# Optimization experiments

Hardware: AMD Instinct MI355X
Metric: run time of the kernel (lower is better)

Reference implementation:

```python
import jax, jax.numpy as jnp
import numpy as np

B, T, NH, MD, FF, HEADS, OUT, PEH = 8, 4096, 16, 64, 256, 4, 1, 32
DH = MD // HEADS

def _ln(x, g, b, eps=1e-5):
    m = jnp.mean(x, -1, keepdims=True)
    v = jnp.mean((x - m) ** 2, -1, keepdims=True)
    return (x - m) * jax.lax.rsqrt(v + eps) * g + b

def _lrelu(x):
    return jax.nn.leaky_relu(x, 0.2)

def setup_inputs():
    key = jax.random.key(0)
    ks = jax.random.split(key, 16)
    w = lambda k, s: jax.random.normal(k, s, jnp.float32) * 0.02
    return dict(
        x=jax.random.normal(ks[0], (B, T, MD), jnp.float32),
        coords1=jax.random.uniform(ks[1], (T,), jnp.float32),
        coords2=jax.random.uniform(ks[2], (T,), jnp.float32),
        g1=jnp.ones((MD,), jnp.float32), be1=jnp.zeros((MD,), jnp.float32),
        Wq=w(ks[3], (MD, MD)), bq=jnp.zeros((MD,), jnp.float32),
        Wk=w(ks[4], (MD, MD)), bk=jnp.zeros((MD,), jnp.float32),
        Wv=w(ks[5], (MD, MD)), bv=jnp.zeros((MD,), jnp.float32),
        logit_scale=jnp.full((HEADS, 1, 1), jnp.log(10.0), jnp.float32),
        Wo=w(ks[6], (MD, MD)), bo=jnp.zeros((MD,), jnp.float32),
        Wp1=w(ks[7], (2, PEH)), bp1=jnp.zeros((PEH,), jnp.float32),
        Wp2=w(ks[8], (PEH, HEADS)), bp2=jnp.zeros((HEADS,), jnp.float32),
        g2=jnp.ones((MD,), jnp.float32), be2=jnp.zeros((MD,), jnp.float32),
        Wn1=w(ks[9], (MD, FF)), bn1=jnp.zeros((FF,), jnp.float32),
        Wn2=w(ks[10], (FF, 1)), bn2=jnp.zeros((1,), jnp.float32),
        g3=jnp.ones((MD * NH,), jnp.float32), be3=jnp.zeros((MD * NH,), jnp.float32),
        Wu1=w(ks[11], (MD * NH, MD * NH)), bu1=jnp.zeros((MD * NH,), jnp.float32),
        Wu2=w(ks[12], (MD * NH, OUT)), bu2=jnp.zeros((OUT,), jnp.float32),
    )

def reference(x, coords1, coords2, g1, be1, Wq, bq, Wk, bk, Wv, bv, logit_scale, Wo, bo,
              Wp1, bp1, Wp2, bp2, g2, be2, Wn1, bn1, Wn2, bn2, g3, be3, Wu1, bu1, Wu2, bu2):
    b, t, e = x.shape
    xn = _ln(x, g1, be1)
    # pairwise relative coords: d[i, j] = c[j] - c[i]  -> [t, t]
    d1 = coords1[None, :] - coords1[:, None]
    d2 = coords2[None, :] - coords2[:, None]
    _, idx = jax.lax.top_k(-(d1 * d1 + d2 * d2), NH)          # [t, nh] kNN indices (incl. self)
    xg = xn[:, idx, :]                                         # [b, t, nh, e] neighbor gather
    c1 = jnp.take_along_axis(d1, idx, axis=1)                  # [t, nh] rel coords of neighbors
    c2 = jnp.take_along_axis(d2, idx, axis=1)
    # relative-position bias among the nh neighbors (shared across batch)
    p = jnp.stack([c1[:, :, None] - c1[:, None, :],
                   c2[:, :, None] - c2[:, None, :]], -1)       # [t, nh, nh, 2]
    bias = _lrelu(p @ Wp1 + bp1) @ Wp2 + bp2                   # [t, nh, nh, H]
    bias = jnp.transpose(bias, (0, 3, 1, 2))                   # [t, H, nh, nh]
    xf = xg.reshape(b * t, NH, e)
    split = lambda z: jnp.transpose(z.reshape(b * t, NH, HEADS, DH), (0, 2, 1, 3))
    qh = split(xf @ Wq + bq)
    kh = split(xf @ Wk + bk)
    vh = split(xf @ Wv + bv)
    # cosine attention with learnable clamped logit scale (SwinV2-style)
    qh = qh / jnp.maximum(jnp.linalg.norm(qh, axis=-1, keepdims=True), 1e-6)
    kh = kh / jnp.maximum(jnp.linalg.norm(kh, axis=-1, keepdims=True), 1e-6)
    scale = jnp.exp(jnp.minimum(logit_scale, jnp.log(100.0)))  # [H,1,1]
    att = jnp.einsum('nhqd,nhkd->nhqk', qh, kh) * scale        # [b*t, H, nh, nh]
    att = att.reshape(b, t, HEADS, NH, NH) + bias[None]
    att = jax.nn.softmax(att, -1).reshape(b * t, HEADS, NH, NH)
    av = jnp.einsum('nhqk,nhkd->nhqd', att, vh)
    av = jnp.transpose(av, (0, 2, 1, 3)).reshape(b * t, NH, e)
    xf = xf + (av @ Wo + bo)                                   # residual 1 (dropout=0)
    xf = _ln(xf, g2, be2)
    xf = xf + _lrelu(_lrelu(xf @ Wn1 + bn1) @ Wn2 + bn2)       # residual 2, [.,.,1] broadcast
    xu = _ln(xf.reshape(b, t, NH * e), g3, be3)                # unfold neighbors
    return _lrelu(_lrelu(xu @ Wu1 + bu1) @ Wu2 + bu2)          # [b, t, OUT]
```

## Files before the change

### kernel.cpp

```cpp
#include <hip/hip_runtime.h>
#include <hip/hip_bf16.h>

#define BB 8
#define TT 4096
#define NHH 16
#define MDD 64
#define FFF 256
#define HEADSS 4
#define DHH 16
#define PEHH 32

#define GM (BB * TT)
#define GK 1024
#define GN 1024
#define BMt 128
#define BNt 128
#define BKt 64
#define NCHUNK (GN / BNt)

#define TOKW 8

typedef float f32x4 __attribute__((ext_vector_type(4)));
typedef short bf16x8 __attribute__((ext_vector_type(8)));

static __device__ __forceinline__ float lrelu(float x) { return x > 0.0f ? x : 0.2f * x; }
static __device__ __forceinline__ unsigned long long umin64(unsigned long long a, unsigned long long b) {
    return a < b ? a : b;
}
static __device__ __forceinline__ unsigned short f2bf(float f) {
    unsigned u = __float_as_uint(f);
    u = u + 0x7fffu + ((u >> 16) & 1u);
    return (unsigned short)(u >> 16);
}
static __device__ __forceinline__ float bf2f(unsigned short u) {
    return __uint_as_float(((unsigned)u) << 16);
}
static __device__ __forceinline__ unsigned pk2(float a, float b) {
    return (unsigned)f2bf(a) | ((unsigned)f2bf(b) << 16);
}
static __device__ __forceinline__ void gload16(const void* g, void* l) {
    __builtin_amdgcn_global_load_lds((const __attribute__((address_space(1))) unsigned int*)g,
                                     (__attribute__((address_space(3))) unsigned int*)l, 16, 0, 0);
}

__global__ __launch_bounds__(256) void k_neighbors(const float* __restrict__ c1,
                                                   const float* __restrict__ c2,
                                                   int* __restrict__ idx,
                                                   float* __restrict__ c1n,
                                                   float* __restrict__ c2n) {
    int t = blockIdx.x;
    int tid = threadIdx.x;
    int lane = tid & 63, w = tid >> 6;
    __shared__ unsigned long long stage[4 * NHH];
    float c1t = c1[t], c2t = c2[t];

    unsigned long long keys[16];
    #pragma unroll
    for (int i = 0; i < 16; ++i) {
        int j = i * 256 + tid;
        float d1 = __fsub_rn(c1[j], c1t);
        float d2 = __fsub_rn(c2[j], c2t);
        float dist = __fadd_rn(__fmul_rn(d1, d1), __fmul_rn(d2, d2));
        keys[i] = (((unsigned long long)__float_as_uint(dist)) << 32) | (unsigned)j;
    }

    #pragma unroll 1
    for (int s = 0; s < NHH; ++s) {
        unsigned long long m = keys[0];
        #pragma unroll
        for (int i = 1; i < 16; ++i) m = umin64(m, keys[i]);
        #pragma unroll
        for (int off = 1; off < 64; off <<= 1)
            m = umin64(m, (unsigned long long)__shfl_xor((long long)m, off));
        #pragma unroll
        for (int i = 0; i < 16; ++i)
            if (keys[i] == m) keys[i] = ~0ull;
        if (lane == 0) stage[w * NHH + s] = m;
    }
    __syncthreads();

    if (w == 0) {
        unsigned long long k0 = stage[lane];
        #pragma unroll 1
        for (int s = 0; s < NHH; ++s) {
            unsigned long long m = k0;
            #pragma unroll
            for (int off = 1; off < 64; off <<= 1)
                m = umin64(m, (unsigned long long)__shfl_xor((long long)m, off));
            if (k0 == m) k0 = ~0ull;
            if (lane == 0) {
                int jj = (int)(unsigned)(m & 0xffffffffu);
                idx[t * NHH + s] = jj;
                c1n[t * NHH + s] = __fsub_rn(c1[jj], c1t);
                c2n[t * NHH + s] = __fsub_rn(c2[jj], c2t);
            }
        }
    }
}

__global__ __launch_bounds__(256) void k_bias(const float* __restrict__ c1n,
                                              const float* __restrict__ c2n,
                                              const float* __restrict__ Wp1,
                                              const float* __restrict__ bp1,
                                              const float* __restrict__ Wp2,
                                              const float* __restrict__ bp2,
                                              float* __restrict__ bias) {
    __shared__ float sWp1[2 * PEHH], sbp1[PEHH], sWp2[PEHH * HEADSS], sbp2[HEADSS];
    int tid = threadIdx.x;
    if (tid < 2 * PEHH) sWp1[tid] = Wp1[tid];
    if (tid < PEHH) sbp1[tid] = bp1[tid];
    if (tid < PEHH * HEADSS) sWp2[tid] = Wp2[tid];
    if (tid < HEADSS) sbp2[tid] = bp2[tid];
    __syncthreads();
    int g = blockIdx.x * 256 + tid;
    if (g >= TT * NHH * NHH) return;
    int j = g & 15, i = (g >> 4) & 15, t = g >> 8;
    float p1 = c1n[t * NHH + i] - c1n[t * NHH + j];
    float p2 = c2n[t * NHH + i] - c2n[t * NHH + j];
    float acc0 = sbp2[0], acc1 = sbp2[1], acc2 = sbp2[2], acc3 = sbp2[3];
    #pragma unroll
    for (int kk = 0; kk < PEHH; ++kk) {
        float h = lrelu(p1 * sWp1[kk] + p2 * sWp1[PEHH + kk] + sbp1[kk]);
        acc0 += h * sWp2[kk * HEADSS + 0];
        acc1 += h * sWp2[kk * HEADSS + 1];
        acc2 += h * sWp2[kk * HEADSS + 2];
        acc3 += h * sWp2[kk * HEADSS + 3];
    }
    float* bt = bias + (size_t)t * HEADSS * NHH * NHH;
    bt[(0 * NHH + i) * NHH + j] = acc0;
    bt[(1 * NHH + i) * NHH + j] = acc1;
    bt[(2 * NHH + i) * NHH + j] = acc2;
    bt[(3 * NHH + i) * NHH + j] = acc3;
}

__global__ __launch_bounds__(256) void k_ln1(const float* __restrict__ x,
                                             const float* __restrict__ g1,
                                             const float* __restrict__ be1,
                                             unsigned short* __restrict__ xn) {
    int row = blockIdx.x * 4 + (threadIdx.x >> 6);
    int lane = threadIdx.x & 63;
    float v = x[(size_t)row * MDD + lane];
    float s = v;
    for (int off = 32; off > 0; off >>= 1) s += __shfl_down(s, off);
    s = __shfl(s, 0);
    float m = s * (1.0f / 64.0f);
    float d = v - m;
    float sq = d * d;
    for (int off = 32; off > 0; off >>= 1) sq += __shfl_down(sq, off);
    sq = __shfl(sq, 0);
    float var = sq * (1.0f / 64.0f);
    float inv = 1.0f / sqrtf(var + 1e-5f);
    xn[(size_t)row * MDD + lane] = f2bf(d * inv * g1[lane] + be1[lane]);
}

__global__ __launch_bounds__(256) void k_prepw(const float* __restrict__ Wq, const float* __restrict__ Wk,
                                               const float* __restrict__ Wv, const float* __restrict__ Wo,
                                               const float* __restrict__ Wn1,
                                               unsigned short* __restrict__ Wall) {
    int id = blockIdx.x * 256 + threadIdx.x;
    int row = id >> 6, kk = id & 63;
    float v;
    if (row < 192) {
        int n = row & 63;
        v = (row < 64) ? Wq[kk * 64 + n] : (row < 128) ? Wk[kk * 64 + n] : Wv[kk * 64 + n];
    } else if (row < 256) {
        v = Wo[kk * 64 + (row - 192)];
    } else {
        v = Wn1[kk * 256 + (row - 256)];
    }
    Wall[row * 64 + ((((kk >> 3) ^ (row & 7)) << 3) | (kk & 7))] = f2bf(v);
}

__global__ __launch_bounds__(512) void k_main(const unsigned short* __restrict__ xnb,
                                              const int* __restrict__ idx,
                                              const float* __restrict__ bias,
                                              const unsigned short* __restrict__ Wall,
                                              const float* __restrict__ bq, const float* __restrict__ bk,
                                              const float* __restrict__ bv, const float* __restrict__ ls,
                                              const float* __restrict__ bo,
                                              const float* __restrict__ g2, const float* __restrict__ be2,
                                              const float* __restrict__ bn1, const float* __restrict__ Wn2,
                                              const float* __restrict__ bn2,
                                              const float* __restrict__ g3, const float* __restrict__ be3,
                                              unsigned short* __restrict__ xu) {
    __shared__ __align__(16) char L[65536 + TOKW * 9216];
    const int tid = threadIdx.x;
    const int lane = tid & 63;
    const int li = lane & 15;
    const int G = lane >> 4;
    const int tok = tid >> 6;
    const int nglob = blockIdx.x * TOKW + tok;
    const int b = nglob >> 12;
    const int t = nglob & (TT - 1);
    const int asw = (li & 7) << 4;

    char* Wl  = L;
    char* xgT = L + 65536 + tok * 9216;
    char* qT  = xgT + 2048;
    char* kT  = xgT + 4096;
    char* vT  = xgT + 6144;

    #pragma unroll
    for (int i = 0; i < 8; ++i) {
        int seg = i * 8 + tok;
        gload16((const char*)Wall + seg * 1024 + lane * 16, Wl + seg * 1024);
    }

    {
        int r16 = lane >> 2, part = lane & 3;
        int j = idx[t * NHH + r16];
        const uint4* sp = reinterpret_cast<const uint4*>(xnb + ((size_t)b * TT + j) * MDD + part * 16);
        uint4 w0 = sp[0], w1 = sp[1];
        int sw = (r16 & 7) << 4;
        *reinterpret_cast<uint4*>(xgT + r16 * 128 + ((part * 32) ^ sw)) = w0;
        *reinterpret_cast<uint4*>(xgT + r16 * 128 + ((part * 32 + 16) ^ sw)) = w1;
    }
    __syncthreads();

    bf16x8 xf0 = *reinterpret_cast<const bf16x8*>(xgT + li * 128 + ((G * 16) ^ asw));
    bf16x8 xf1 = *reinterpret_cast<const bf16x8*>(xgT + li * 128 + ((64 + G * 16) ^ asw));
    f32x4 acc[12];
    #pragma unroll
    for (int mt = 0; mt < 12; ++mt) {
        const char* wr = Wl + (mt * 16 + li) * 128;
        bf16x8 w0 = *reinterpret_cast<const bf16x8*>(wr + ((G * 16) ^ asw));
        bf16x8 w1 = *reinterpret_cast<const bf16x8*>(wr + ((64 + G * 16) ^ asw));
        f32x4 a = (f32x4){0.0f, 0.0f, 0.0f, 0.0f};
        a = __builtin_amdgcn_mfma_f32_16x16x32_bf16(w0, xf0, a, 0, 0, 0);
        a = __builtin_amdgcn_mfma_f32_16x16x32_bf16(w1, xf1, a, 0, 0, 0);
        acc[mt] = a;
    }
    #pragma unroll
    for (int h = 0; h < 4; ++h) {
        float4 b4 = *reinterpret_cast<const float4*>(bq + h * 16 + G * 4);
        float q0 = acc[h][0] + b4.x, q1 = acc[h][1] + b4.y, q2 = acc[h][2] + b4.z, q3 = acc[h][3] + b4.w;
        float sq = q0 * q0 + q1 * q1 + q2 * q2 + q3 * q3;
        sq += __shfl_xor(sq, 16); sq += __shfl_xor(sq, 32);
        float iq = 1.0f / fmaxf(sqrtf(sq), 1e-6f);
        uint2 u; u.x = pk2(q0 * iq, q1 * iq); u.y = pk2(q2 * iq, q3 * iq);
        *reinterpret_cast<uint2*>(qT + li * 128 + ((h * 32 + G * 8) ^ asw)) = u;
    }
    #pragma unroll
    for (int h = 0; h < 4; ++h) {
        float4 b4 = *reinterpret_cast<const float4*>(bk + h * 16 + G * 4);
        float k0 = acc[4 + h][0] + b4.x, k1 = acc[4 + h][1] + b4.y, k2 = acc[4 + h][2] + b4.z, k3 = acc[4 + h][3] + b4.w;
        float sk = k0 * k0 + k1 * k1 + k2 * k2 + k3 * k3;
        sk += __shfl_xor(sk, 16); sk += __shfl_xor(sk, 32);
        float ik = 1.0f / fmaxf(sqrtf(sk), 1e-6f);
        uint2 u; u.x = pk2(k0 * ik, k1 * ik); u.y = pk2(k2 * ik, k3 * ik);
        *reinterpret_cast<uint2*>(kT + li * 128 + ((h * 32 + G * 8) ^ asw)) = u;
    }
    #pragma unroll
    for (int m2 = 0; m2 < 4; ++m2) {
        float4 b4 = *reinterpret_cast<const float4*>(bv + m2 * 16 + G * 4);
        float v0 = acc[8 + m2][0] + b4.x, v1 = acc[8 + m2][1] + b4.y, v2 = acc[8 + m2][2] + b4.z, v3 = acc[8 + m2][3] + b4.w;
        int c0 = m2 * 16 + G * 4;
        *reinterpret_cast<unsigned short*>(vT + (c0 + 0) * 48 + li * 2) = f2bf(v0);
        *reinterpret_cast<unsigned short*>(vT + (c0 + 1) * 48 + li * 2) = f2bf(v1);
        *reinterpret_cast<unsigned short*>(vT + (c0 + 2) * 48 + li * 2) = f2bf(v2);
        *reinterpret_cast<unsigned short*>(vT + (c0 + 3) * 48 + li * 2) = f2bf(v3);
    }

    float lsa[4] = {ls[0], ls[1], ls[2], ls[3]};

    #pragma unroll
    for (int h = 0; h < 4; ++h) {
        bf16x8 kf8 = {}, qf8 = {};
        if (G < 2) {
            kf8 = *reinterpret_cast<const bf16x8*>(kT + li * 128 + ((h * 32 + G * 16) ^ asw));
            qf8 = *reinterpret_cast<const bf16x8*>(qT + li * 128 + ((h * 32 + G * 16) ^ asw));
        }
        f32x4 s4 = __builtin_amdgcn_mfma_f32_16x16x32_bf16(kf8, qf8, (f32x4){0.0f, 0.0f, 0.0f, 0.0f}, 0, 0, 0);
        float sch = __expf(fminf(lsa[h], 4.60517018598809136804f));
        const float4 b4 = *reinterpret_cast<const float4*>(bias + ((size_t)t * 4 + h) * 256 + li * 16 + G * 4);
        float a0 = s4[0] * sch + b4.x;
        float a1 = s4[1] * sch + b4.y;
        float a2 = s4[2] * sch + b4.z;
        float a3 = s4[3] * sch + b4.w;
        float mx = fmaxf(fmaxf(a0, a1), fmaxf(a2, a3));
        mx = fmaxf(mx, __shfl_xor(mx, 16));
        mx = fmaxf(mx, __shfl_xor(mx, 32));
        float e0 = __expf(a0 - mx), e1 = __expf(a1 - mx), e2 = __expf(a2 - mx), e3 = __expf(a3 - mx);
        float sm = e0 + e1 + e2 + e3;
        sm += __shfl_xor(sm, 16);
        sm += __shfl_xor(sm, 32);
        float inv = 1.0f / sm;
        e0 *= inv; e1 *= inv; e2 *= inv; e3 *= inv;
        unsigned p01 = pk2(e0, e1), p23 = pk2(e2, e3);
        int s0l = li + 32 * (G & 1);
        uint4 pw;
        pw.x = (unsigned)__shfl((int)p01, s0l);
        pw.y = (unsigned)__shfl((int)p23, s0l);
        pw.z = (unsigned)__shfl((int)p01, s0l + 16);
        pw.w = (unsigned)__shfl((int)p23, s0l + 16);
        if (G >= 2) { pw.x = 0; pw.y = 0; pw.z = 0; pw.w = 0; }
        bf16x8 vf8 = {};
        if (G < 2) vf8 = *reinterpret_cast<const bf16x8*>(vT + (h * 16 + li) * 48 + G * 16);
        f32x4 pv = __builtin_amdgcn_mfma_f32_16x16x32_bf16(vf8, __builtin_bit_cast(bf16x8, pw),
                                                           (f32x4){0.0f, 0.0f, 0.0f, 0.0f}, 0, 0, 0);
        uint2 u; u.x = pk2(pv[0], pv[1]); u.y = pk2(pv[2], pv[3]);
        *reinterpret_cast<uint2*>(qT + li * 128 + ((h * 32 + G * 8) ^ asw)) = u;
    }

    float xfn[4][4];
    float rowadd;
    {
        bf16x8 av0 = *reinterpret_cast<const bf16x8*>(qT + li * 128 + ((G * 16) ^ asw));
        bf16x8 av1 = *reinterpret_cast<const bf16x8*>(qT + li * 128 + ((64 + G * 16) ^ asw));
        f32x4 oac[4];
        #pragma unroll
        for (int mt = 0; mt < 4; ++mt) {
            const char* wr = Wl + (192 + mt * 16 + li) * 128;
            bf16x8 w0 = *reinterpret_cast<const bf16x8*>(wr + ((G * 16) ^ asw));
            bf16x8 w1 = *reinterpret_cast<const bf16x8*>(wr + ((64 + G * 16) ^ asw));
            f32x4 a = (f32x4){0.0f, 0.0f, 0.0f, 0.0f};
            a = __builtin_amdgcn_mfma_f32_16x16x32_bf16(w0, av0, a, 0, 0, 0);
            a = __builtin_amdgcn_mfma_f32_16x16x32_bf16(w1, av1, a, 0, 0, 0);
            oac[mt] = a;
        }
        float xf[4][4];
        float s = 0.0f, sq = 0.0f;
        #pragma unroll
        for (int mt = 0; mt < 4; ++mt) {
            float4 bo4 = *reinterpret_cast<const float4*>(bo + mt * 16 + G * 4);
            uint2 xg2 = *reinterpret_cast<const uint2*>(xgT + li * 128 + ((mt * 32 + G * 8) ^ asw));
            float r0 = bf2f((unsigned short)(xg2.x & 0xffffu));
            float r1 = bf2f((unsigned short)(xg2.x >> 16));
            float r2 = bf2f((unsigned short)(xg2.y & 0xffffu));
            float r3 = bf2f((unsigned short)(xg2.y >> 16));
            xf[mt][0] = oac[mt][0] + bo4.x + r0;
            xf[mt][1] = oac[mt][1] + bo4.y + r1;
            xf[mt][2] = oac[mt][2] + bo4.z + r2;
            xf[mt][3] = oac[mt][3] + bo4.w + r3;
            #pragma unroll
            for (int r = 0; r < 4; ++r) { s += xf[mt][r]; sq += xf[mt][r] * xf[mt][r]; }
        }
        s += __shfl_xor(s, 16); s += __shfl_xor(s, 32);
        sq += __shfl_xor(sq, 16); sq += __shfl_xor(sq, 32);
        float m = s * (1.0f / 64.0f);
        float var = sq * (1.0f / 64.0f) - m * m;
        float inv = 1.0f / sqrtf(var + 1e-5f);
        #pragma unroll
        for (int mt = 0; mt < 4; ++mt) {
            float4 g24 = *reinterpret_cast<const float4*>(g2 + mt * 16 + G * 4);
            float4 be24 = *reinterpret_cast<const float4*>(be2 + mt * 16 + G * 4);
            xfn[mt][0] = (xf[mt][0] - m) * inv * g24.x + be24.x;
            xfn[mt][1] = (xf[mt][1] - m) * inv * g24.y + be24.y;
            xfn[mt][2] = (xf[mt][2] - m) * inv * g24.z + be24.z;
            xfn[mt][3] = (xf[mt][3] - m) * inv * g24.w + be24.w;
            uint2 u; u.x = pk2(xfn[mt][0], xfn[mt][1]); u.y = pk2(xfn[mt][2], xfn[mt][3]);
            *reinterpret_cast<uint2*>(kT + li * 128 + ((mt * 32 + G * 8) ^ asw)) = u;
        }
    }

    {
        bf16x8 xn0 = *reinterpret_cast<const bf16x8*>(kT + li * 128 + ((G * 16) ^ asw));
        bf16x8 xn1 = *reinterpret_cast<const bf16x8*>(kT + li * 128 + ((64 + G * 16) ^ asw));
        float dot = 0.0f;
        #pragma unroll
        for (int mt = 0; mt < 16; ++mt) {
            const char* wr = Wl + (256 + mt * 16 + li) * 128;
            bf16x8 w0 = *reinterpret_cast<const bf16x8*>(wr + ((G * 16) ^ asw));
            bf16x8 w1 = *reinterpret_cast<const bf16x8*>(wr + ((64 + G * 16) ^ asw));
            f32x4 a = (f32x4){0.0f, 0.0f, 0.0f, 0.0f};
            a = __builtin_amdgcn_mfma_f32_16x16x32_bf16(w0, xn0, a, 0, 0, 0);
            a = __builtin_amdgcn_mfma_f32_16x16x32_bf16(w1, xn1, a, 0, 0, 0);
            float4 bn14 = *reinterpret_cast<const float4*>(bn1 + mt * 16 + G * 4);
            float4 w24 = *reinterpret_cast<const float4*>(Wn2 + mt * 16 + G * 4);
            dot += lrelu(a[0] + bn14.x) * w24.x;
            dot += lrelu(a[1] + bn14.y) * w24.y;
            dot += lrelu(a[2] + bn14.z) * w24.z;
            dot += lrelu(a[3] + bn14.w) * w24.w;
        }
        dot += __shfl_xor(dot, 16);
        dot += __shfl_xor(dot, 32);
        rowadd = lrelu(dot + bn2[0]);
    }

    {
        float s = 0.0f, sq = 0.0f;
        float vals[4][4];
        #pragma unroll
        for (int mt = 0; mt < 4; ++mt)
            #pragma unroll
            for (int r = 0; r < 4; ++r) {
                float v = xfn[mt][r] + rowadd;
                vals[mt][r] = v;
                s += v; sq += v * v;
            }
        s += __shfl_xor(s, 1); s += __shfl_xor(s, 2); s += __shfl_xor(s, 4);
        s += __shfl_xor(s, 8); s += __shfl_xor(s, 16); s += __shfl_xor(s, 32);
        sq += __shfl_xor(sq, 1); sq += __shfl_xor(sq, 2); sq += __shfl_xor(sq, 4);
        sq += __shfl_xor(sq, 8); sq += __shfl_xor(sq, 16); sq += __shfl_xor(sq, 32);
        float m = s * (1.0f / 1024.0f);
        float var = sq * (1.0f / 1024.0f) - m * m;
        float inv = 1.0f / sqrtf(var + 1e-5f);
        int swm = nglob & 7;
        #pragma unroll
        for (int mt = 0; mt < 4; ++mt) {
            int o0 = li * 64 + mt * 16 + G * 4;
            float4 g34 = *reinterpret_cast<const float4*>(g3 + o0);
            float4 be34 = *reinterpret_cast<const float4*>(be3 + o0);
            float u0 = (vals[mt][0] - m) * inv * g34.x + be34.x;
            float u1 = (vals[mt][1] - m) * inv * g34.y + be34.y;
            float u2 = (vals[mt][2] - m) * inv * g34.z + be34.z;
            float u3 = (vals[mt][3] - m) * inv * g34.w + be34.w;
            uint2 u; u.x = pk2(u0, u1); u.y = pk2(u2, u3);
            size_t p = (size_t)nglob * 1024 + li * 64
                     + ((((mt * 2 + (G >> 1)) ^ swm) << 3) | ((G & 1) * 4));
            *reinterpret_cast<uint2*>(xu + p) = u;
        }
    }
}

__global__ __launch_bounds__(256) void k_cvtW(const float* __restrict__ W,
                                              unsigned short* __restrict__ Wt) {
    __shared__ float tile[32][33];
    int tk = blockIdx.x & 31;
    int tn = blockIdx.x >> 5;
    int c = threadIdx.x & 31, r4 = threadIdx.x >> 5;
    #pragma unroll
    for (int p = 0; p < 4; ++p) {
        int r = p * 8 + r4;
        tile[r][c] = W[(size_t)(tk * 32 + r) * GN + tn * 32 + c];
    }
    __syncthreads();
    #pragma unroll
    for (int p = 0; p < 4; ++p) {
        int r = p * 8 + r4;
        int n = tn * 32 + r;
        int kk = tk * 32 + c;
        int chunk = kk >> 6, slot = (kk >> 3) & 7, e = kk & 7;
        Wt[(size_t)n * GK + chunk * 64 + ((slot ^ (n & 7)) << 3) + e] = f2bf(tile[c][r]);
    }
}

__global__ __launch_bounds__(256) void k_gemm(const unsigned short* __restrict__ xu,
                                              const unsigned short* __restrict__ Wt,
                                              const float* __restrict__ bu1,
                                              const float* __restrict__ Wu2,
                                              float* __restrict__ partial) {
    int bm = blockIdx.x;
    int bn = blockIdx.y;
    int tid = threadIdx.x;
    int w = tid >> 6, l = tid & 63;
    int wm = w >> 1, wn = w & 1;
    int lr = l & 15, lg = l >> 4;

    __shared__ __align__(1024) unsigned short LB[4 * BMt * BKt];
    __shared__ float rowpart[2][BMt];
    char* base = reinterpret_cast<char*>(LB);

    f32x4 acc[4][4];
    #pragma unroll
    for (int i = 0; i < 4; ++i)
        #pragma unroll
        for (int j = 0; j < 4; ++j)
            acc[i][j] = (f32x4){0.0f, 0.0f, 0.0f, 0.0f};

    const size_t arow = (size_t)(bm * BMt) * GK;
    const size_t brow = (size_t)(bn * BNt) * GK;

    #define STAGE(kt, buf)                                                            \
        {                                                                             \
            char* Ab_ = base + (buf) * 32768;                                         \
            char* Bb_ = Ab_ + 16384;                                                  \
            int k0_ = (kt) * BKt;                                                     \
            _Pragma("unroll")                                                         \
            for (int p = 0; p < 4; ++p) {                                             \
                int seg = w * 4 + p;                                                  \
                int rl = seg * 8 + (l >> 3);                                          \
                gload16(xu + arow + (size_t)rl * GK + k0_ + (l & 7) * 8, Ab_ + seg * 1024); \
                gload16(Wt + brow + (size_t)rl * GK + k0_ + (l & 7) * 8, Bb_ + seg * 1024); \
            }                                                                         \
        }

    STAGE(0, 0)
    __syncthreads();

    for (int kt = 0; kt < GK / BKt; ++kt) {
        int buf = kt & 1;
        if (kt < GK / BKt - 1) STAGE(kt + 1, buf ^ 1)
        char* Ab = base + buf * 32768;
        char* Bb = Ab + 16384;
        #pragma unroll
        for (int ks = 0; ks < 2; ++ks) {
            bf16x8 af[4], bfr[4];
            #pragma unroll
            for (int rf = 0; rf < 4; ++rf) {
                int row = wm * 64 + rf * 16 + lr;
                int coff = (ks * 64 + lg * 16) ^ ((row & 7) << 4);
                af[rf] = *reinterpret_cast<const bf16x8*>(Ab + row * 128 + coff);
            }
            #pragma unroll
            for (int nf = 0; nf < 4; ++nf) {
                int rowb = wn * 64 + nf * 16 + lr;
                int coff = (ks * 64 + lg * 16) ^ ((rowb & 7) << 4);
                bfr[nf] = *reinterpret_cast<const bf16x8*>(Bb + rowb * 128 + coff);
            }
            #pragma unroll
            for (int rf = 0; rf < 4; ++rf)
                #pragma unroll
                for (int nf = 0; nf < 4; ++nf)
                    acc[rf][nf] = __builtin_amdgcn_mfma_f32_16x16x32_bf16(af[rf], bfr[nf], acc[rf][nf], 0, 0, 0);
        }
        __syncthreads();
    }
    #undef STAGE

    float b1v[4], w2v[4];
    #pragma unroll
    for (int nf = 0; nf < 4; ++nf) {
        int nn = bn * BNt + wn * 64 + nf * 16 + lr;
        b1v[nf] = bu1[nn];
        w2v[nf] = Wu2[nn];
    }
    float rowsum[4][4];
    #pragma unroll
    for (int rf = 0; rf < 4; ++rf) {
        #pragma unroll
        for (int j = 0; j < 4; ++j) {
            float s = 0.0f;
            #pragma unroll
            for (int nf = 0; nf < 4; ++nf)
                s += lrelu(acc[rf][nf][j] + b1v[nf]) * w2v[nf];
            #pragma unroll
            for (int off = 1; off < 16; off <<= 1)
                s += __shfl_xor(s, off);
            rowsum[rf][j] = s;
        }
    }
    if (lr == 0) {
        #pragma unroll
        for (int rf = 0; rf < 4; ++rf)
            #pragma unroll
            for (int j = 0; j < 4; ++j)
                rowpart[wn][wm * 64 + rf * 16 + lg * 4 + j] = rowsum[rf][j];
    }
    __syncthreads();
    if (tid < BMt) {
        float v = rowpart[0][tid] + rowpart[1][tid];
        partial[((size_t)(bm * BMt + tid)) * NCHUNK + bn] = v;
    }
}

__global__ __launch_bounds__(256) void k_reduce(const float* __restrict__ partial,
                                                const float* __restrict__ bu2,
                                                float* __restrict__ out) {
    int m = blockIdx.x * 256 + threadIdx.x;
    float s = bu2[0];
    #pragma unroll
    for (int c = 0; c < NCHUNK; ++c) s += partial[(size_t)m * NCHUNK + c];
    out[m] = lrelu(s);
}

extern "C" void kernel_launch(void* const* d_in, const int* in_sizes, int n_in,
                              void* d_out, int out_size, void* d_ws, size_t ws_size,
                              hipStream_t stream) {
    const float* x   = (const float*)d_in[0];
    const float* c1  = (const float*)d_in[1];
    const float* c2  = (const float*)d_in[2];
    const float* g1  = (const float*)d_in[3];
    const float* be1 = (const float*)d_in[4];
    const float* Wq  = (const float*)d_in[5];
    const float* bq  = (const float*)d_in[6];
    const float* Wk  = (const float*)d_in[7];
    const float* bk  = (const float*)d_in[8];
    const float* Wv  = (const float*)d_in[9];
    const float* bv  = (const float*)d_in[10];
    const float* ls  = (const float*)d_in[11];
    const float* Wo  = (const float*)d_in[12];
    const float* bo  = (const float*)d_in[13];
    const float* Wp1 = (const float*)d_in[14];
    const float* bp1 = (const float*)d_in[15];
    const float* Wp2 = (const float*)d_in[16];
    const float* bp2 = (const float*)d_in[17];
    const float* g2  = (const float*)d_in[18];
    const float* be2 = (const float*)d_in[19];
    const float* Wn1 = (const float*)d_in[20];
    const float* bn1 = (const float*)d_in[21];
    const float* Wn2 = (const float*)d_in[22];
    const float* bn2 = (const float*)d_in[23];
    const float* g3  = (const float*)d_in[24];
    const float* be3 = (const float*)d_in[25];
    const float* Wu1 = (const float*)d_in[26];
    const float* bu1 = (const float*)d_in[27];
    const float* Wu2 = (const float*)d_in[28];
    const float* bu2 = (const float*)d_in[29];
    float* out = (float*)d_out;

    char* ws = (char*)d_ws;
    size_t off = 0;
    int*   idx  = (int*)(ws + off);   off += (size_t)TT * NHH * 4;
    float* c1n  = (float*)(ws + off); off += (size_t)TT * NHH * 4;
    float* c2n  = (float*)(ws + off); off += (size_t)TT * NHH * 4;
    float* bias = (float*)(ws + off); off += (size_t)TT * HEADSS * NHH * NHH * 4;
    unsigned short* xnb  = (unsigned short*)(ws + off); off += (size_t)BB * TT * MDD * 2;
    unsigned short* xuB  = (unsigned short*)(ws + off); off += (size_t)GM * GK * 2;
    unsigned short* Wu1t = (unsigned short*)(ws + off); off += (size_t)GK * GN * 2;
    float* partial = (float*)(ws + off); off += (size_t)GM * NCHUNK * 4;
    unsigned short* Wall = (unsigned short*)(ws + off); off += 512 * 64 * 2;

    k_neighbors<<<TT, 256, 0, stream>>>(c1, c2, idx, c1n, c2n);
    k_bias<<<(TT * NHH * NHH + 255) / 256, 256, 0, stream>>>(c1n, c2n, Wp1, bp1, Wp2, bp2, bias);
    k_ln1<<<(BB * TT) / 4, 256, 0, stream>>>(x, g1, be1, xnb);
    k_prepw<<<128, 256, 0, stream>>>(Wq, Wk, Wv, Wo, Wn1, Wall);
    k_cvtW<<<1024, 256, 0, stream>>>(Wu1, Wu1t);
    k_main<<<(BB * TT) / TOKW, 512, 0, stream>>>(xnb, idx, bias, Wall,
                                                 bq, bk, bv, ls, bo, g2, be2, bn1, Wn2, bn2, g3, be3, xuB);
    k_gemm<<<dim3(GM / BMt, GN / BNt), 256, 0, stream>>>(xuB, Wu1t, bu1, Wu2, partial);
    k_reduce<<<GM / 256, 256, 0, stream>>>(partial, bu2, out);
}
```

Measured before the change: 358.7 us.

## Read prepacked MFMA weight fragments from global memory instead of staging in LDS

The weight prep kernel now packs Wq/Wk/Wv/Wo/Wn1 into per-lane MFMA fragment order, so each lane loads its bf16x8 operand directly from global memory (served from L1/L2) rather than every block copying 64 KB of weights into LDS. This removes the per-block 64 KB LDS fill and the block-wide barrier, and shrinks LDS per block so more blocks fit per CU. Blocks shrink to 4 tokens and 256 threads with launch_bounds(256,4) to raise occupancy. The cost is repeated global/cache loads of weights on every MFMA step, which adds load latency and cache traffic.

Measured after the change: 338.8 us. -5.6%, faster.

```diff
diff --git a/kernel.cpp b/kernel.cpp
--- a/kernel.cpp
+++ b/kernel.cpp
@@ -18,7 +18,7 @@
 #define BKt 64
 #define NCHUNK (GN / BNt)
 
-#define TOKW 8
+#define TOKW 4
 
 typedef float f32x4 __attribute__((ext_vector_type(4)));
 typedef short bf16x8 __attribute__((ext_vector_type(8)));
@@ -158,20 +158,33 @@
                                                const float* __restrict__ Wn1,
                                                unsigned short* __restrict__ Wall) {
     int id = blockIdx.x * 256 + threadIdx.x;
-    int row = id >> 6, kk = id & 63;
+    int f = id >> 9;
+    int w = (id >> 3) & 63;
+    int e = id & 7;
+    int li = w & 15, G = w >> 4;
     float v;
-    if (row < 192) {
-        int n = row & 63;
-        v = (row < 64) ? Wq[kk * 64 + n] : (row < 128) ? Wk[kk * 64 + n] : Wv[kk * 64 + n];
-    } else if (row < 256) {
-        v = Wo[kk * 64 + (row - 192)];
+    if (f < 24) {
+        int mt = f >> 1, ks = f & 1;
+        int n = mt * 16 + li;
+        int k = ks * 32 + G * 8 + e;
+        v = (n < 64) ? Wq[k * 64 + n] : (n < 128) ? Wk[k * 64 + (n - 64)] : Wv[k * 64 + (n - 128)];
+    } else if (f < 32) {
+        int g2i = f - 24;
+        int mt = g2i >> 1, ks = g2i & 1;
+        int n = mt * 16 + li;
+        int k = ks * 32 + G * 8 + e;
+        v = Wo[k * 64 + n];
     } else {
-        v = Wn1[kk * 256 + (row - 256)];
-    }
-    Wall[row * 64 + ((((kk >> 3) ^ (row & 7)) << 3) | (kk & 7))] = f2bf(v);
-}
-
-__global__ __launch_bounds__(512) void k_main(const unsigned short* __restrict__ xnb,
+        int g2i = f - 32;
+        int mt = g2i >> 1, ks = g2i & 1;
+        int n = mt * 16 + li;
+        int k = ks * 32 + G * 8 + e;
+        v = Wn1[k * 256 + n];
+    }
+    Wall[id] = f2bf(v);
+}
+
+__global__ __launch_bounds__(256, 4) void k_main(const unsigned short* __restrict__ xnb,
                                               const int* __restrict__ idx,
                                               const float* __restrict__ bias,
                                               const unsigned short* __restrict__ Wall,
@@ -183,7 +196,7 @@
                                               const float* __restrict__ bn2,
                                               const float* __restrict__ g3, const float* __restrict__ be3,
                                               unsigned short* __restrict__ xu) {
-    __shared__ __align__(16) char L[65536 + TOKW * 9216];
+    __shared__ __align__(16) char L[TOKW * 9216];
     const int tid = threadIdx.x;
     const int lane = tid & 63;
     const int li = lane & 15;
@@ -194,17 +207,10 @@
     const int t = nglob & (TT - 1);
     const int asw = (li & 7) << 4;
 
-    char* Wl  = L;
-    char* xgT = L + 65536 + tok * 9216;
+    char* xgT = L + tok * 9216;
     char* qT  = xgT + 2048;
     char* kT  = xgT + 4096;
     char* vT  = xgT + 6144;
-
-    #pragma unroll
-    for (int i = 0; i < 8; ++i) {
-        int seg = i * 8 + tok;
-        gload16((const char*)Wall + seg * 1024 + lane * 16, Wl + seg * 1024);
-    }
 
     {
         int r16 = lane >> 2, part = lane & 3;
@@ -215,16 +221,14 @@
         *reinterpret_cast<uint4*>(xgT + r16 * 128 + ((part * 32) ^ sw)) = w0;
         *reinterpret_cast<uint4*>(xgT + r16 * 128 + ((part * 32 + 16) ^ sw)) = w1;
     }
-    __syncthreads();
 
     bf16x8 xf0 = *reinterpret_cast<const bf16x8*>(xgT + li * 128 + ((G * 16) ^ asw));
     bf16x8 xf1 = *reinterpret_cast<const bf16x8*>(xgT + li * 128 + ((64 + G * 16) ^ asw));
     f32x4 acc[12];
     #pragma unroll
     for (int mt = 0; mt < 12; ++mt) {
-        const char* wr = Wl + (mt * 16 + li) * 128;
-        bf16x8 w0 = *reinterpret_cast<const bf16x8*>(wr + ((G * 16) ^ asw));
-        bf16x8 w1 = *reinterpret_cast<const bf16x8*>(wr + ((64 + G * 16) ^ asw));
+        bf16x8 w0 = *reinterpret_cast<const bf16x8*>(Wall + (mt * 2 + 0) * 512 + lane * 8);
+        bf16x8 w1 = *reinterpret_cast<const bf16x8*>(Wall + (mt * 2 + 1) * 512 + lane * 8);
         f32x4 a = (f32x4){0.0f, 0.0f, 0.0f, 0.0f};
         a = __builtin_amdgcn_mfma_f32_16x16x32_bf16(w0, xf0, a, 0, 0, 0);
         a = __builtin_amdgcn_mfma_f32_16x16x32_bf16(w1, xf1, a, 0, 0, 0);
@@ -310,9 +314,8 @@
         f32x4 oac[4];
         #pragma unroll
         for (int mt = 0; mt < 4; ++mt) {
-            const char* wr = Wl + (192 + mt * 16 + li) * 128;
-            bf16x8 w0 = *reinterpret_cast<const bf16x8*>(wr + ((G * 16) ^ asw));
-            bf16x8 w1 = *reinterpret_cast<const bf16x8*>(wr + ((64 + G * 16) ^ asw));
+            bf16x8 w0 = *reinterpret_cast<const bf16x8*>(Wall + (24 + mt * 2 + 0) * 512 + lane * 8);
+            bf16x8 w1 = *reinterpret_cast<const bf16x8*>(Wall + (24 + mt * 2 + 1) * 512 + lane * 8);
             f32x4 a = (f32x4){0.0f, 0.0f, 0.0f, 0.0f};
             a = __builtin_amdgcn_mfma_f32_16x16x32_bf16(w0, av0, a, 0, 0, 0);
             a = __builtin_amdgcn_mfma_f32_16x16x32_bf16(w1, av1, a, 0, 0, 0);
@@ -359,9 +362,8 @@
         float dot = 0.0f;
         #pragma unroll
         for (int mt = 0; mt < 16; ++mt) {
-            const char* wr = Wl + (256 + mt * 16 + li) * 128;
-            bf16x8 w0 = *reinterpret_cast<const bf16x8*>(wr + ((G * 16) ^ asw));
-            bf16x8 w1 = *reinterpret_cast<const bf16x8*>(wr + ((64 + G * 16) ^ asw));
+            bf16x8 w0 = *reinterpret_cast<const bf16x8*>(Wall + (32 + mt * 2 + 0) * 512 + lane * 8);
+            bf16x8 w1 = *reinterpret_cast<const bf16x8*>(Wall + (32 + mt * 2 + 1) * 512 + lane * 8);
             f32x4 a = (f32x4){0.0f, 0.0f, 0.0f, 0.0f};
             a = __builtin_amdgcn_mfma_f32_16x16x32_bf16(w0, xn0, a, 0, 0, 0);
             a = __builtin_amdgcn_mfma_f32_16x16x32_bf16(w1, xn1, a, 0, 0, 0);
@@ -599,14 +601,14 @@
     unsigned short* xuB  = (unsigned short*)(ws + off); off += (size_t)GM * GK * 2;
     unsigned short* Wu1t = (unsigned short*)(ws + off); off += (size_t)GK * GN * 2;
     float* partial = (float*)(ws + off); off += (size_t)GM * NCHUNK * 4;
-    unsigned short* Wall = (unsigned short*)(ws + off); off += 512 * 64 * 2;
+    unsigned short* Wall = (unsigned short*)(ws + off); off += 64 * 1024;
 
     k_neighbors<<<TT, 256, 0, stream>>>(c1, c2, idx, c1n, c2n);
     k_bias<<<(TT * NHH * NHH + 255) / 256, 256, 0, stream>>>(c1n, c2n, Wp1, bp1, Wp2, bp2, bias);
     k_ln1<<<(BB * TT) / 4, 256, 0, stream>>>(x, g1, be1, xnb);
     k_prepw<<<128, 256, 0, stream>>>(Wq, Wk, Wv, Wo, Wn1, Wall);
     k_cvtW<<<1024, 256, 0, stream>>>(Wu1, Wu1t);
-    k_main<<<(BB * TT) / TOKW, 512, 0, stream>>>(xnb, idx, bias, Wall,
+    k_main<<<(BB * TT) / TOKW, 256, 0, stream>>>(xnb, idx, bias, Wall,
                                                  bq, bk, bv, ls, bo, g2, be2, bn1, Wn2, bn2, g3, be3, xuB);
     k_gemm<<<dim3(GM / BMt, GN / BNt), 256, 0, stream>>>(xuB, Wu1t, bu1, Wu2, partial);
     k_reduce<<<GM / 256, 256, 0, stream>>>(partial, bu2, out);
```
